# Kernel tuning notes

Measured on AMD Instinct MI355X. Metric: run time of the kernel, lower is better.

Reference implementation:

```python
import jax, jax.numpy as jnp
import numpy as np

D = 256    # lstm_encoder_size
B = 1024   # batch (number of agents/trajectories)
T = 512    # prediction horizon (recurrence steps)
EPS = 1e-5


def setup_inputs() -> dict:
    key = jax.random.key(0)
    k = jax.random.split(key, 10)
    s = 1.0 / np.sqrt(D)
    return {
        "KS_ALL": jax.random.normal(k[0], (1, B, D), jnp.float32),
        "next_vf": jax.random.normal(k[1], (B, T), jnp.float32),
        # Koopman operators (torch Linear stores [out, in]; no bias)
        "A_w": jax.random.normal(k[2], (D, D), jnp.float32) * (0.4 * s),  # contractive
        "B_w": jax.random.normal(k[3], (D, 1), jnp.float32) * s,
        # decoder params (liner_dec=False)
        "W0": jax.random.normal(k[4], (2 * D, D), jnp.float32) * s,
        "b0": jnp.zeros((2 * D,), jnp.float32),
        "W1": jax.random.normal(k[5], (D, 2 * D), jnp.float32) / np.sqrt(2.0 * D),
        "b1": jnp.zeros((D,), jnp.float32),
        "ln_g": jnp.ones((D,), jnp.float32),
        "ln_b": jnp.zeros((D,), jnp.float32),
        "W2": jax.random.normal(k[6], (D, D), jnp.float32) * s,
        "b2": jnp.zeros((D,), jnp.float32),
        "W3": jax.random.normal(k[7], (3, D), jnp.float32) * s,
        "b3": jnp.zeros((3,), jnp.float32),
    }


def _layer_norm(x, g, b):
    mu = jnp.mean(x, axis=-1, keepdims=True)
    var = jnp.var(x, axis=-1, keepdims=True)
    return (x - mu) * jax.lax.rsqrt(var + EPS) * g + b


def reference(KS_ALL, next_vf, A_w, B_w, W0, b0, W1, b1, ln_g, ln_b, W2, b2, W3, b3):
    # train_flag=True -> use only the first time slice of KS_ALL
    ks0 = KS_ALL[0]                 # [B, D]
    u = next_vf.T                   # [T, B] time-major, matches permute(1,0,2)
    b_vec = B_w[:, 0]               # [D]  (Linear(1, D) on scalar input)

    def step(ks, u_t):
        ks_new = ks @ A_w.T + u_t[:, None] * b_vec[None, :]  # [B, D]
        return ks_new, ks_new

    _, ks_seq = jax.lax.scan(step, ks0, u)                   # [T, B, D]
    KS_pre = jnp.concatenate([ks0[None], ks_seq], axis=0)    # [T+1, B, D]

    # nonlinear decoder (eval mode: dropout is identity; use_elu=True)
    s1 = jnp.tanh(KS_pre @ W0.T + b0)          # [T+1, B, 2D]
    s2 = jnp.tanh(s1 @ W1.T + b1)              # [T+1, B, D]
    s2 = _layer_norm(KS_pre + s2, ln_g, ln_b)  # AddAndNorm
    s3 = jax.nn.elu(s2 @ W2.T + b2)
    OS = s3 @ W3.T + b3                        # [T+1, B, 3]
    return KS_pre, OS
```

## Files before the change

### kernel.cpp

```cpp
#include <hip/hip_runtime.h>

typedef unsigned short u16;
typedef __attribute__((ext_vector_type(8))) short bf16x8;
typedef __attribute__((ext_vector_type(4))) short bf16x4;
typedef __attribute__((ext_vector_type(4))) float f32x4;

#define MFMA16(a, b, c) __builtin_amdgcn_mfma_f32_16x16x32_bf16((a), (b), (c), 0, 0, 0)

#define OFF_U8   0
#define U8_CPY   598016
#define OFF_KS0  4784128
#define OFF_W0   5046272
#define OFF_W1   5177344
#define OFF_W2   5308416
#define OFF_CRT  5373952
#define OFF_P    5390336
#define OS_OFF   134479872

__device__ __forceinline__ u16 f2bf(float f) {
  union { float f; unsigned int i; } v; v.f = f;
  return (u16)((v.i + 0x7fffu + ((v.i >> 16) & 1u)) >> 16);
}
__device__ __forceinline__ float bf2f(u16 u) {
  union { unsigned int i; float f; } v; v.i = ((unsigned int)u) << 16;
  return v.f;
}
__device__ __forceinline__ float fast_tanh(float x) {
  float e = __expf(2.0f * x);
  return 1.0f - __fdividef(2.0f, e + 1.0f);
}

__global__ void k_prep(const float* __restrict__ KS_ALL, const float* __restrict__ next_vf,
                       const float* __restrict__ A_w, const float* __restrict__ W0,
                       const float* __restrict__ W1, const float* __restrict__ W2,
                       u16* __restrict__ ws) {
  int idx = blockIdx.x * 256 + threadIdx.x;
  if (idx < 4784128) {
    int p = idx / U8_CPY;
    int rem = idx - p * U8_CPY;
    int b = rem / 584;
    int c = rem - b * 584;
    int col = c + p;
    ws[OFF_U8 + idx] = (col >= 64 && col < 576) ? f2bf(next_vf[b * 512 + col - 64]) : (u16)0;
    return;
  }
  idx -= 4784128;
  if (idx < 262144) { ws[OFF_KS0 + idx] = f2bf(KS_ALL[idx]); return; }
  idx -= 262144;
  if (idx < 131072) { ws[OFF_W0 + idx] = f2bf(W0[idx]); return; }
  idx -= 131072;
  if (idx < 131072) { ws[OFF_W1 + idx] = f2bf(W1[idx]); return; }
  idx -= 131072;
  if (idx < 65536)  { ws[OFF_W2 + idx] = f2bf(W2[idx]); return; }
  idx -= 65536;
  if (idx < 65536) {
    int r = idx >> 8, c = idx & 255;
    ws[OFF_P + idx] = (r == c) ? (u16)0x3F80 : (u16)0;
    ws[OFF_P + 65536 + idx] = f2bf(A_w[idx]);
  }
}

__global__ __launch_bounds__(512) void k_pow(u16* __restrict__ ws, int s) {
  const u16* P = ws + OFF_P;
  int j = blockIdx.y + 1;
  int mh = blockIdx.x;
  int lane = threadIdx.x & 63, w = threadIdx.x >> 6;
  int wm = w >> 2, wn = w & 3;
  int lg = lane >> 4, ll = lane & 15;
  const u16* Am = P + s * 65536;
  const u16* Bm = P + j * 65536;
  f32x4 acc[4][4];
  f32x4 z = {0.f, 0.f, 0.f, 0.f};
#pragma unroll
  for (int mi = 0; mi < 4; ++mi)
#pragma unroll
    for (int ni = 0; ni < 4; ++ni) acc[mi][ni] = z;
#pragma unroll
  for (int ks = 0; ks < 8; ++ks) {
    bf16x8 a[4], b[4];
    int kk = ks * 32 + lg * 8;
#pragma unroll
    for (int mi = 0; mi < 4; ++mi) {
      int row = mh * 128 + wm * 64 + mi * 16 + ll;
      a[mi] = *(const bf16x8*)(Am + row * 256 + kk);
    }
#pragma unroll
    for (int ni = 0; ni < 4; ++ni) {
      int col = wn * 64 + ni * 16 + ll;
#pragma unroll
      for (int e = 0; e < 8; ++e) b[ni][e] = (short)Bm[(kk + e) * 256 + col];
    }
#pragma unroll
    for (int mi = 0; mi < 4; ++mi)
#pragma unroll
      for (int ni = 0; ni < 4; ++ni) acc[mi][ni] = MFMA16(a[mi], b[ni], acc[mi][ni]);
  }
  u16* Pd = ws + OFF_P + (s + j) * 65536;
#pragma unroll
  for (int mi = 0; mi < 4; ++mi)
#pragma unroll
    for (int ni = 0; ni < 4; ++ni)
#pragma unroll
      for (int r = 0; r < 4; ++r) {
        int row = mh * 128 + wm * 64 + mi * 16 + lg * 4 + r;
        int col = wn * 64 + ni * 16 + ll;
        Pd[row * 256 + col] = f2bf(acc[mi][ni][r]);
      }
}

__global__ void k_crevt(const float* __restrict__ B_w, u16* __restrict__ ws) {
  int s = blockIdx.x;
  int n = threadIdx.x;
  const u16* Pr = ws + OFF_P + (63 - s) * 65536 + n * 256;
  float acc = 0.f;
  for (int k = 0; k < 256; ++k) acc += bf2f(Pr[k]) * B_w[k];
  ws[OFF_CRT + n * 64 + s] = f2bf(acc);
}

__global__ __launch_bounds__(512) void k_ks(const u16* __restrict__ ws, float* __restrict__ out) {
  __shared__ __align__(16) float Hf[32 * 260];
  const int t  = blockIdx.y;
  const int R0 = blockIdx.x * 64;
  const int tid = threadIdx.x;
  const int lane = tid & 63, w = tid >> 6;
  const int lg = lane >> 4, ll = lane & 15;
  f32x4 z = {0.f, 0.f, 0.f, 0.f};

  f32x4 acc[4][2];
#pragma unroll
  for (int mi = 0; mi < 4; ++mi)
#pragma unroll
    for (int ni = 0; ni < 2; ++ni) acc[mi][ni] = z;
  {
    const u16* CrevT = ws + OFF_CRT;
    const u16* u8b = ws + OFF_U8 + (size_t)(t & 7) * U8_CPY + (t & ~7);
#pragma unroll
    for (int ksu = 0; ksu < 2; ++ksu) {
      bf16x8 au[4];
#pragma unroll
      for (int mi = 0; mi < 4; ++mi)
        au[mi] = *(const bf16x8*)(u8b + (R0 + mi * 16 + ll) * 584 + ksu * 32 + lg * 8);
#pragma unroll
      for (int ni = 0; ni < 2; ++ni) {
        int n = w * 32 + ni * 16 + ll;
        bf16x8 bfr = *(const bf16x8*)(CrevT + n * 64 + ksu * 32 + lg * 8);
#pragma unroll
        for (int mi = 0; mi < 4; ++mi) acc[mi][ni] = MFMA16(au[mi], bfr, acc[mi][ni]);
      }
    }
    if (t < 64) {
      const u16* Pt = ws + OFF_P + t * 65536;
      const u16* ks0b = ws + OFF_KS0;
#pragma unroll
      for (int ks = 0; ks < 8; ++ks) {
        bf16x8 a[4], b[2];
#pragma unroll
        for (int mi = 0; mi < 4; ++mi)
          a[mi] = *(const bf16x8*)(ks0b + (R0 + mi * 16 + ll) * 256 + ks * 32 + lg * 8);
#pragma unroll
        for (int ni = 0; ni < 2; ++ni)
          b[ni] = *(const bf16x8*)(Pt + (w * 32 + ni * 16 + ll) * 256 + ks * 32 + lg * 8);
#pragma unroll
        for (int mi = 0; mi < 4; ++mi)
#pragma unroll
          for (int ni = 0; ni < 2; ++ni) acc[mi][ni] = MFMA16(a[mi], b[ni], acc[mi][ni]);
      }
    }
  }
#pragma unroll 1
  for (int p = 0; p < 2; ++p) {
#pragma unroll
    for (int mi2 = 0; mi2 < 2; ++mi2) {
      int mi = p * 2 + mi2;
#pragma unroll
      for (int ni = 0; ni < 2; ++ni)
#pragma unroll
        for (int r = 0; r < 4; ++r)
          Hf[(mi2 * 16 + lg * 4 + r) * 260 + w * 32 + ni * 16 + ll] = acc[mi][ni][r];
    }
    __syncthreads();
    float* ob = out + (size_t)t * 262144 + (size_t)(R0 + p * 32) * 256;
#pragma unroll
    for (int it = 0; it < 4; ++it) {
      int idx = it * 512 + tid;
      int row = idx >> 6, c4 = idx & 63;
      f32x4 v = *(const f32x4*)(Hf + row * 260 + c4 * 4);
      __builtin_nontemporal_store(v, (f32x4*)(ob + row * 256 + c4 * 4));
    }
    __syncthreads();
  }
}

__global__ __launch_bounds__(512) void k_mlp(const u16* __restrict__ ws,
                                             const float* __restrict__ outf,
                                             const float* __restrict__ b0,
                                             const float* __restrict__ b1,
                                             const float* __restrict__ lng,
                                             const float* __restrict__ lnb,
                                             const float* __restrict__ b2,
                                             const float* __restrict__ W3,
                                             const float* __restrict__ b3,
                                             float* __restrict__ out) {
  __shared__ __align__(16) u16 Xb[16896];
  __shared__ __align__(16) u16 Hs[8448];
  __shared__ float par[2308];
  __shared__ float osb[208];
  float* pb0 = par;
  float* pb1 = par + 512;
  float* pg  = par + 768;
  float* pbt = par + 1024;
  float* pb2 = par + 1280;
  float* pW3 = par + 1536;
  float* pb3 = par + 2304;
  const int t  = blockIdx.y;
  const int R0 = blockIdx.x * 64;
  const int tid = threadIdx.x;
  const int lane = tid & 63, w = tid >> 6;
  const int lg = lane >> 4, ll = lane & 15;
  f32x4 z = {0.f, 0.f, 0.f, 0.f};

  pb0[tid] = b0[tid];
  if (tid < 256) { pb1[tid] = b1[tid]; pg[tid] = lng[tid]; pbt[tid] = lnb[tid]; pb2[tid] = b2[tid]; }
  if (tid < 512) pW3[tid] = W3[tid];
  if (tid < 256) pW3[512 + tid] = W3[512 + tid];
  if (tid < 4) pb3[tid] = (tid < 3) ? b3[tid] : 0.f;

  {
    const float* xs = outf + (size_t)t * 262144 + (size_t)R0 * 256;
#pragma unroll
    for (int it = 0; it < 8; ++it) {
      int idx = it * 512 + tid;
      int row = idx >> 6, c4 = idx & 63;
      f32x4 v = __builtin_nontemporal_load((const f32x4*)(xs + row * 256 + c4 * 4));
      bf16x4 h;
#pragma unroll
      for (int e = 0; e < 4; ++e) h[e] = (short)f2bf(v[e]);
      int byt = (((row << 9) + ((c4 >> 1) << 4)) ^ ((row & 7) << 4)) + ((c4 & 1) << 3);
      *(bf16x4*)(Xb + (byt >> 1)) = h;
    }
  }
  __syncthreads();

  const u16* W0b = ws + OFF_W0;
  const u16* W1b = ws + OFF_W1;
  f32x4 accL2[4][2];
#pragma unroll
  for (int mi = 0; mi < 4; ++mi)
#pragma unroll
    for (int ni = 0; ni < 2; ++ni) accL2[mi][ni] = z;
  const int colL1 = w * 16 + ll;
#pragma unroll 1
  for (int q = 0; q < 4; ++q) {
    f32x4 accQ[4];
#pragma unroll
    for (int mi = 0; mi < 4; ++mi) accQ[mi] = z;
#pragma unroll
    for (int ks = 0; ks < 8; ++ks) {
      bf16x8 b = *(const bf16x8*)(W0b + (q * 128 + colL1) * 256 + ks * 32 + lg * 8);
#pragma unroll
      for (int mi = 0; mi < 4; ++mi) {
        int rl = mi * 16 + ll;
        int byt = ((rl << 9) + ks * 64 + (lg << 4)) ^ ((rl & 7) << 4);
        bf16x8 a = *(const bf16x8*)(Xb + (byt >> 1));
        accQ[mi] = MFMA16(a, b, accQ[mi]);
      }
    }
#pragma unroll
    for (int mi = 0; mi < 4; ++mi)
#pragma unroll
      for (int r = 0; r < 4; ++r) {
        int rl2 = mi * 16 + lg * 4 + r;
        float v = fast_tanh(accQ[mi][r] + pb0[q * 128 + colL1]);
        int byt = ((rl2 << 8) + (colL1 << 1)) ^ ((rl2 & 7) << 4);
        Hs[byt >> 1] = f2bf(v);
      }
    __syncthreads();
#pragma unroll
    for (int ks2 = 0; ks2 < 4; ++ks2) {
      bf16x8 bf0 = *(const bf16x8*)(W1b + (w * 32 + ll) * 512 + q * 128 + ks2 * 32 + lg * 8);
      bf16x8 bf1 = *(const bf16x8*)(W1b + (w * 32 + 16 + ll) * 512 + q * 128 + ks2 * 32 + lg * 8);
#pragma unroll
      for (int mi = 0; mi < 4; ++mi) {
        int rl = mi * 16 + ll;
        int byt = ((rl << 8) + ks2 * 64 + (lg << 4)) ^ ((rl & 7) << 4);
        bf16x8 a = *(const bf16x8*)(Hs + (byt >> 1));
        accL2[mi][0] = MFMA16(a, bf0, accL2[mi][0]);
        accL2[mi][1] = MFMA16(a, bf1, accL2[mi][1]);
      }
    }
    __syncthreads();
  }

#pragma unroll
  for (int mi = 0; mi < 4; ++mi)
#pragma unroll
    for (int ni = 0; ni < 2; ++ni)
#pragma unroll
      for (int r = 0; r < 4; ++r) {
        int rl = mi * 16 + lg * 4 + r;
        int col = w * 32 + ni * 16 + ll;
        int bx = ((rl << 9) + (col << 1)) ^ ((rl & 7) << 4);
        float v = bf2f(Xb[bx >> 1]) + fast_tanh(accL2[mi][ni][r] + pb1[col]);
        Xb[bx >> 1] = f2bf(v);
      }
  __syncthreads();

  {
    int row = tid >> 3, jq = tid & 7;
    bf16x8 chv[4];
    int byts[4];
#pragma unroll
    for (int q = 0; q < 4; ++q) {
      byts[q] = ((row << 9) + ((jq * 32 + q * 8) << 1)) ^ ((row & 7) << 4);
      chv[q] = *(const bf16x8*)(Xb + (byts[q] >> 1));
    }
    float s = 0.f, ss = 0.f;
#pragma unroll
    for (int q = 0; q < 4; ++q)
#pragma unroll
      for (int e = 0; e < 8; ++e) { float v = bf2f((u16)chv[q][e]); s += v; ss += v * v; }
    s += __shfl_xor(s, 1);  s += __shfl_xor(s, 2);  s += __shfl_xor(s, 4);
    ss += __shfl_xor(ss, 1); ss += __shfl_xor(ss, 2); ss += __shfl_xor(ss, 4);
    float mu = s * 0.00390625f;
    float var = ss * 0.00390625f - mu * mu;
    float rstd = rsqrtf(var + 1e-5f);
#pragma unroll
    for (int q = 0; q < 4; ++q) {
      bf16x8 o;
#pragma unroll
      for (int e = 0; e < 8; ++e) {
        int col = jq * 32 + q * 8 + e;
        float v = (bf2f((u16)chv[q][e]) - mu) * rstd * pg[col] + pbt[col];
        o[e] = (short)f2bf(v);
      }
      *(bf16x8*)(Xb + (byts[q] >> 1)) = o;
    }
  }
  __syncthreads();

  f32x4 a3[4][2];
#pragma unroll
  for (int mi = 0; mi < 4; ++mi)
#pragma unroll
    for (int ni = 0; ni < 2; ++ni) a3[mi][ni] = z;
  {
    const u16* W2b = ws + OFF_W2;
#pragma unroll
    for (int ks = 0; ks < 8; ++ks) {
      bf16x8 bf0 = *(const bf16x8*)(W2b + (w * 32 + ll) * 256 + ks * 32 + lg * 8);
      bf16x8 bf1 = *(const bf16x8*)(W2b + (w * 32 + 16 + ll) * 256 + ks * 32 + lg * 8);
#pragma unroll
      for (int mi = 0; mi < 4; ++mi) {
        int rl = mi * 16 + ll;
        int byt = ((rl << 9) + ks * 64 + (lg << 4)) ^ ((rl & 7) << 4);
        bf16x8 a = *(const bf16x8*)(Xb + (byt >> 1));
        a3[mi][0] = MFMA16(a, bf0, a3[mi][0]);
        a3[mi][1] = MFMA16(a, bf1, a3[mi][1]);
      }
    }
  }
  __syncthreads();
#pragma unroll
  for (int mi = 0; mi < 4; ++mi)
#pragma unroll
    for (int ni = 0; ni < 2; ++ni)
#pragma unroll
      for (int r = 0; r < 4; ++r) {
        int rl = mi * 16 + lg * 4 + r;
        int col = w * 32 + ni * 16 + ll;
        float v = a3[mi][ni][r] + pb2[col];
        v = v > 0.f ? v : (__expf(v) - 1.f);
        Xb[rl * 264 + col] = f2bf(v);
      }
  __syncthreads();

  {
    int row = tid >> 3, jq = tid & 7;
    const u16* xr = Xb + row * 264 + jq * 32;
    float d0 = 0.f, d1 = 0.f, d2 = 0.f;
#pragma unroll
    for (int q = 0; q < 4; ++q) {
      bf16x8 c = *(const bf16x8*)(xr + q * 8);
#pragma unroll
      for (int e = 0; e < 8; ++e) {
        float v = bf2f((u16)c[e]);
        int col = jq * 32 + q * 8 + e;
        d0 += v * pW3[col]; d1 += v * pW3[256 + col]; d2 += v * pW3[512 + col];
      }
    }
    d0 += __shfl_xor(d0, 1); d0 += __shfl_xor(d0, 2); d0 += __shfl_xor(d0, 4);
    d1 += __shfl_xor(d1, 1); d1 += __shfl_xor(d1, 2); d1 += __shfl_xor(d1, 4);
    d2 += __shfl_xor(d2, 1); d2 += __shfl_xor(d2, 2); d2 += __shfl_xor(d2, 4);
    if (jq == 0) {
      osb[row * 3]     = d0 + pb3[0];
      osb[row * 3 + 1] = d1 + pb3[1];
      osb[row * 3 + 2] = d2 + pb3[2];
    }
  }
  __syncthreads();
  if (tid < 48) {
    f32x4 v = *(const f32x4*)(osb + tid * 4);
    __builtin_nontemporal_store(v, (f32x4*)(out + OS_OFF + (size_t)t * 3072 + (size_t)R0 * 3 + tid * 4));
  }
}

extern "C" void kernel_launch(void* const* d_in, const int* in_sizes, int n_in,
                              void* d_out, int out_size, void* d_ws, size_t ws_size,
                              hipStream_t stream) {
  const float* KS_ALL  = (const float*)d_in[0];
  const float* next_vf = (const float*)d_in[1];
  const float* A_w     = (const float*)d_in[2];
  const float* B_w     = (const float*)d_in[3];
  const float* W0      = (const float*)d_in[4];
  const float* b0      = (const float*)d_in[5];
  const float* W1      = (const float*)d_in[6];
  const float* b1      = (const float*)d_in[7];
  const float* lng     = (const float*)d_in[8];
  const float* lnb     = (const float*)d_in[9];
  const float* W2      = (const float*)d_in[10];
  const float* b2      = (const float*)d_in[11];
  const float* W3      = (const float*)d_in[12];
  const float* b3      = (const float*)d_in[13];
  u16* ws = (u16*)d_ws;
  float* out = (float*)d_out;

  k_prep<<<21248, 256, 0, stream>>>(KS_ALL, next_vf, A_w, W0, W1, W2, ws);
  for (int s = 1; s <= 32; s <<= 1)
    k_pow<<<dim3(2, s), 512, 0, stream>>>(ws, s);
  k_crevt<<<64, 256, 0, stream>>>(B_w, ws);

  k_ks<<<dim3(16, 513), 512, 0, stream>>>(ws, out);
  k_mlp<<<dim3(16, 513), 512, 0, stream>>>(ws, out, b0, b1, lng, lnb, b2, W3, b3, out);
}
```

Measured before the change: 1.503 ms.

## Double k_mlp block to 1024 threads, halving per-wave columns and L1 chunks

The decoder MLP kernel now launches 1024 threads (16 waves) per 64-row tile instead of 512. Each wave owns 16 output columns instead of 32, and the hidden layer is processed in two 256-wide chunks instead of four 128-wide chunks, with a larger shared staging buffer. The LayerNorm and final projection reductions are respread over 16 lanes per row. The aim is more waves in flight per tile to hide latency and fewer barrier rounds, at the cost of fewer accumulators per wave, more shared memory and possibly lower block occupancy per CU.

```diff
diff --git a/kernel.cpp b/kernel.cpp
--- a/kernel.cpp
+++ b/kernel.cpp
@@ -191,18 +191,18 @@
   }
 }
 
-__global__ __launch_bounds__(512) void k_mlp(const u16* __restrict__ ws,
-                                             const float* __restrict__ outf,
-                                             const float* __restrict__ b0,
-                                             const float* __restrict__ b1,
-                                             const float* __restrict__ lng,
-                                             const float* __restrict__ lnb,
-                                             const float* __restrict__ b2,
-                                             const float* __restrict__ W3,
-                                             const float* __restrict__ b3,
-                                             float* __restrict__ out) {
+__global__ __launch_bounds__(1024) void k_mlp(const u16* __restrict__ ws,
+                                              const float* __restrict__ outf,
+                                              const float* __restrict__ b0,
+                                              const float* __restrict__ b1,
+                                              const float* __restrict__ lng,
+                                              const float* __restrict__ lnb,
+                                              const float* __restrict__ b2,
+                                              const float* __restrict__ W3,
+                                              const float* __restrict__ b3,
+                                              float* __restrict__ out) {
   __shared__ __align__(16) u16 Xb[16896];
-  __shared__ __align__(16) u16 Hs[8448];
+  __shared__ __align__(16) u16 Hs[16384];
   __shared__ float par[2308];
   __shared__ float osb[208];
   float* pb0 = par;
@@ -217,19 +217,19 @@
   const int tid = threadIdx.x;
   const int lane = tid & 63, w = tid >> 6;
   const int lg = lane >> 4, ll = lane & 15;
+  const int colW = w * 16 + ll;
   f32x4 z = {0.f, 0.f, 0.f, 0.f};
 
-  pb0[tid] = b0[tid];
+  if (tid < 512) pb0[tid] = b0[tid];
   if (tid < 256) { pb1[tid] = b1[tid]; pg[tid] = lng[tid]; pbt[tid] = lnb[tid]; pb2[tid] = b2[tid]; }
-  if (tid < 512) pW3[tid] = W3[tid];
-  if (tid < 256) pW3[512 + tid] = W3[512 + tid];
+  if (tid < 768) pW3[tid] = W3[tid];
   if (tid < 4) pb3[tid] = (tid < 3) ? b3[tid] : 0.f;
 
   {
     const float* xs = outf + (size_t)t * 262144 + (size_t)R0 * 256;
 #pragma unroll
-    for (int it = 0; it < 8; ++it) {
-      int idx = it * 512 + tid;
+    for (int it = 0; it < 4; ++it) {
+      int idx = it * 1024 + tid;
       int row = idx >> 6, c4 = idx & 63;
       f32x4 v = __builtin_nontemporal_load((const f32x4*)(xs + row * 256 + c4 * 4));
       bf16x4 h;
@@ -243,20 +243,17 @@
 
   const u16* W0b = ws + OFF_W0;
   const u16* W1b = ws + OFF_W1;
-  f32x4 accL2[4][2];
-#pragma unroll
-  for (int mi = 0; mi < 4; ++mi)
-#pragma unroll
-    for (int ni = 0; ni < 2; ++ni) accL2[mi][ni] = z;
-  const int colL1 = w * 16 + ll;
+  f32x4 accL2[4];
+#pragma unroll
+  for (int mi = 0; mi < 4; ++mi) accL2[mi] = z;
 #pragma unroll 1
-  for (int q = 0; q < 4; ++q) {
+  for (int q = 0; q < 2; ++q) {
     f32x4 accQ[4];
 #pragma unroll
     for (int mi = 0; mi < 4; ++mi) accQ[mi] = z;
 #pragma unroll
     for (int ks = 0; ks < 8; ++ks) {
-      bf16x8 b = *(const bf16x8*)(W0b + (q * 128 + colL1) * 256 + ks * 32 + lg * 8);
+      bf16x8 b = *(const bf16x8*)(W0b + (q * 256 + colW) * 256 + ks * 32 + lg * 8);
 #pragma unroll
       for (int mi = 0; mi < 4; ++mi) {
         int rl = mi * 16 + ll;
@@ -270,22 +267,20 @@
 #pragma unroll
       for (int r = 0; r < 4; ++r) {
         int rl2 = mi * 16 + lg * 4 + r;
-        float v = fast_tanh(accQ[mi][r] + pb0[q * 128 + colL1]);
-        int byt = ((rl2 << 8) + (colL1 << 1)) ^ ((rl2 & 7) << 4);
+        float v = fast_tanh(accQ[mi][r] + pb0[q * 256 + colW]);
+        int byt = ((rl2 << 9) + (colW << 1)) ^ ((rl2 & 7) << 4);
         Hs[byt >> 1] = f2bf(v);
       }
     __syncthreads();
 #pragma unroll
-    for (int ks2 = 0; ks2 < 4; ++ks2) {
-      bf16x8 bf0 = *(const bf16x8*)(W1b + (w * 32 + ll) * 512 + q * 128 + ks2 * 32 + lg * 8);
-      bf16x8 bf1 = *(const bf16x8*)(W1b + (w * 32 + 16 + ll) * 512 + q * 128 + ks2 * 32 + lg * 8);
+    for (int ks = 0; ks < 8; ++ks) {
+      bf16x8 b = *(const bf16x8*)(W1b + colW * 512 + q * 256 + ks * 32 + lg * 8);
 #pragma unroll
       for (int mi = 0; mi < 4; ++mi) {
         int rl = mi * 16 + ll;
-        int byt = ((rl << 8) + ks2 * 64 + (lg << 4)) ^ ((rl & 7) << 4);
+        int byt = ((rl << 9) + ks * 64 + (lg << 4)) ^ ((rl & 7) << 4);
         bf16x8 a = *(const bf16x8*)(Hs + (byt >> 1));
-        accL2[mi][0] = MFMA16(a, bf0, accL2[mi][0]);
-        accL2[mi][1] = MFMA16(a, bf1, accL2[mi][1]);
+        accL2[mi] = MFMA16(a, b, accL2[mi]);
       }
     }
     __syncthreads();
@@ -294,68 +289,59 @@
 #pragma unroll
   for (int mi = 0; mi < 4; ++mi)
 #pragma unroll
-    for (int ni = 0; ni < 2; ++ni)
-#pragma unroll
-      for (int r = 0; r < 4; ++r) {
-        int rl = mi * 16 + lg * 4 + r;
-        int col = w * 32 + ni * 16 + ll;
-        int bx = ((rl << 9) + (col << 1)) ^ ((rl & 7) << 4);
-        float v = bf2f(Xb[bx >> 1]) + fast_tanh(accL2[mi][ni][r] + pb1[col]);
-        Xb[bx >> 1] = f2bf(v);
-      }
+    for (int r = 0; r < 4; ++r) {
+      int rl = mi * 16 + lg * 4 + r;
+      int bx = ((rl << 9) + (colW << 1)) ^ ((rl & 7) << 4);
+      float v = bf2f(Xb[bx >> 1]) + fast_tanh(accL2[mi][r] + pb1[colW]);
+      Xb[bx >> 1] = f2bf(v);
+    }
   __syncthreads();
 
   {
-    int row = tid >> 3, jq = tid & 7;
-    bf16x8 chv[4];
-    int byts[4];
-#pragma unroll
-    for (int q = 0; q < 4; ++q) {
-      byts[q] = ((row << 9) + ((jq * 32 + q * 8) << 1)) ^ ((row & 7) << 4);
-      chv[q] = *(const bf16x8*)(Xb + (byts[q] >> 1));
-    }
+    int row = tid >> 4, jq = tid & 15;
+    bf16x8 chv[2];
+    int byt0 = ((row << 9) + ((jq * 16) << 1)) ^ ((row & 7) << 4);
+    int byt1 = ((row << 9) + ((jq * 16 + 8) << 1)) ^ ((row & 7) << 4);
+    chv[0] = *(const bf16x8*)(Xb + (byt0 >> 1));
+    chv[1] = *(const bf16x8*)(Xb + (byt1 >> 1));
     float s = 0.f, ss = 0.f;
 #pragma unroll
-    for (int q = 0; q < 4; ++q)
+    for (int q = 0; q < 2; ++q)
 #pragma unroll
       for (int e = 0; e < 8; ++e) { float v = bf2f((u16)chv[q][e]); s += v; ss += v * v; }
-    s += __shfl_xor(s, 1);  s += __shfl_xor(s, 2);  s += __shfl_xor(s, 4);
-    ss += __shfl_xor(ss, 1); ss += __shfl_xor(ss, 2); ss += __shfl_xor(ss, 4);
+    s += __shfl_xor(s, 1);  s += __shfl_xor(s, 2);  s += __shfl_xor(s, 4);  s += __shfl_xor(s, 8);
+    ss += __shfl_xor(ss, 1); ss += __shfl_xor(ss, 2); ss += __shfl_xor(ss, 4); ss += __shfl_xor(ss, 8);
     float mu = s * 0.00390625f;
     float var = ss * 0.00390625f - mu * mu;
     float rstd = rsqrtf(var + 1e-5f);
 #pragma unroll
-    for (int q = 0; q < 4; ++q) {
+    for (int q = 0; q < 2; ++q) {
       bf16x8 o;
 #pragma unroll
       for (int e = 0; e < 8; ++e) {
-        int col = jq * 32 + q * 8 + e;
+        int col = jq * 16 + q * 8 + e;
         float v = (bf2f((u16)chv[q][e]) - mu) * rstd * pg[col] + pbt[col];
         o[e] = (short)f2bf(v);
       }
-      *(bf16x8*)(Xb + (byts[q] >> 1)) = o;
-    }
-  }
-  __syncthreads();
-
-  f32x4 a3[4][2];
-#pragma unroll
-  for (int mi = 0; mi < 4; ++mi)
-#pragma unroll
-    for (int ni = 0; ni < 2; ++ni) a3[mi][ni] = z;
+      *(bf16x8*)(Xb + ((q ? byt1 : byt0) >> 1)) = o;
+    }
+  }
+  __syncthreads();
+
+  f32x4 a3[4];
+#pragma unroll
+  for (int mi = 0; mi < 4; ++mi) a3[mi] = z;
   {
     const u16* W2b = ws + OFF_W2;
 #pragma unroll
     for (int ks = 0; ks < 8; ++ks) {
-      bf16x8 bf0 = *(const bf16x8*)(W2b + (w * 32 + ll) * 256 + ks * 32 + lg * 8);
-      bf16x8 bf1 = *(const bf16x8*)(W2b + (w * 32 + 16 + ll) * 256 + ks * 32 + lg * 8);
+      bf16x8 b = *(const bf16x8*)(W2b + colW * 256 + ks * 32 + lg * 8);
 #pragma unroll
       for (int mi = 0; mi < 4; ++mi) {
         int rl = mi * 16 + ll;
         int byt = ((rl << 9) + ks * 64 + (lg << 4)) ^ ((rl & 7) << 4);
         bf16x8 a = *(const bf16x8*)(Xb + (byt >> 1));
-        a3[mi][0] = MFMA16(a, bf0, a3[mi][0]);
-        a3[mi][1] = MFMA16(a, bf1, a3[mi][1]);
+        a3[mi] = MFMA16(a, b, a3[mi]);
       }
     }
   }
@@ -363,34 +349,31 @@
 #pragma unroll
   for (int mi = 0; mi < 4; ++mi)
 #pragma unroll
-    for (int ni = 0; ni < 2; ++ni)
-#pragma unroll
-      for (int r = 0; r < 4; ++r) {
-        int rl = mi * 16 + lg * 4 + r;
-        int col = w * 32 + ni * 16 + ll;
-        float v = a3[mi][ni][r] + pb2[col];
-        v = v > 0.f ? v : (__expf(v) - 1.f);
-        Xb[rl * 264 + col] = f2bf(v);
-      }
+    for (int r = 0; r < 4; ++r) {
+      int rl = mi * 16 + lg * 4 + r;
+      float v = a3[mi][r] + pb2[colW];
+      v = v > 0.f ? v : (__expf(v) - 1.f);
+      Xb[rl * 264 + colW] = f2bf(v);
+    }
   __syncthreads();
 
   {
-    int row = tid >> 3, jq = tid & 7;
-    const u16* xr = Xb + row * 264 + jq * 32;
+    int row = tid >> 4, jq = tid & 15;
+    const u16* xr = Xb + row * 264 + jq * 16;
     float d0 = 0.f, d1 = 0.f, d2 = 0.f;
 #pragma unroll
-    for (int q = 0; q < 4; ++q) {
+    for (int q = 0; q < 2; ++q) {
       bf16x8 c = *(const bf16x8*)(xr + q * 8);
 #pragma unroll
       for (int e = 0; e < 8; ++e) {
         float v = bf2f((u16)c[e]);
-        int col = jq * 32 + q * 8 + e;
+        int col = jq * 16 + q * 8 + e;
         d0 += v * pW3[col]; d1 += v * pW3[256 + col]; d2 += v * pW3[512 + col];
       }
     }
-    d0 += __shfl_xor(d0, 1); d0 += __shfl_xor(d0, 2); d0 += __shfl_xor(d0, 4);
-    d1 += __shfl_xor(d1, 1); d1 += __shfl_xor(d1, 2); d1 += __shfl_xor(d1, 4);
-    d2 += __shfl_xor(d2, 1); d2 += __shfl_xor(d2, 2); d2 += __shfl_xor(d2, 4);
+    d0 += __shfl_xor(d0, 1); d0 += __shfl_xor(d0, 2); d0 += __shfl_xor(d0, 4); d0 += __shfl_xor(d0, 8);
+    d1 += __shfl_xor(d1, 1); d1 += __shfl_xor(d1, 2); d1 += __shfl_xor(d1, 4); d1 += __shfl_xor(d1, 8);
+    d2 += __shfl_xor(d2, 1); d2 += __shfl_xor(d2, 2); d2 += __shfl_xor(d2, 4); d2 += __shfl_xor(d2, 8);
     if (jq == 0) {
       osb[row * 3]     = d0 + pb3[0];
       osb[row * 3 + 1] = d1 + pb3[1];
@@ -430,5 +413,5 @@
   k_crevt<<<64, 256, 0, stream>>>(B_w, ws);
 
   k_ks<<<dim3(16, 513), 512, 0, stream>>>(ws, out);
-  k_mlp<<<dim3(16, 513), 512, 0, stream>>>(ws, out, b0, b1, lng, lnb, b2, W3, b3, out);
-}
+  k_mlp<<<dim3(16, 513), 1024, 0, stream>>>(ws, out, b0, b1, lng, lnb, b2, W3, b3, out);
+}
```

New measurement: 1.453 ms. -3.3%, faster.

## Fuse first decoder layer into KS kernel and chunk time to stream hidden activations

Applied to the files above, without the earlier changes.

The KS computation kernel now also runs the first decoder GEMM and tanh from the bf16 KS tile held in shared memory. It writes the bf16 hidden layer to a workspace buffer instead of having the MLP kernel re-read the fp32 KS output. The second kernel handles layers 2-4 from that buffer. The work is split into four time chunks so the intermediate buffer stays small and may stay cache-resident between the paired kernels. The cost is heavier per-block shared memory, extra launches, and a round trip of the 512-wide hidden layer through global memory.

```diff
diff --git a/kernel.cpp b/kernel.cpp
--- a/kernel.cpp
+++ b/kernel.cpp
@@ -15,6 +15,7 @@
 #define OFF_W2   5308416
 #define OFF_CRT  5373952
 #define OFF_P    5390336
+#define OFF_H1   9650176
 #define OS_OFF   134479872
 
 __device__ __forceinline__ u16 f2bf(float f) {
@@ -117,15 +118,25 @@
   ws[OFF_CRT + n * 64 + s] = f2bf(acc);
 }
 
-__global__ __launch_bounds__(512) void k_ks(const u16* __restrict__ ws, float* __restrict__ out) {
-  __shared__ __align__(16) float Hf[32 * 260];
-  const int t  = blockIdx.y;
+__global__ __launch_bounds__(512) void k_ksl1(const u16* __restrict__ ws,
+                                              const float* __restrict__ b0,
+                                              u16* __restrict__ h1,
+                                              float* __restrict__ out, int t0) {
+  __shared__ __align__(16) u16 Xb[16896];
+  __shared__ __align__(16) unsigned char Hraw[33792];
+  __shared__ float pb0s[512];
+  float* Hf = (float*)Hraw;
+  u16* Hb = (u16*)Hraw;
+  const int by = blockIdx.y;
+  const int t  = t0 + by;
   const int R0 = blockIdx.x * 64;
   const int tid = threadIdx.x;
   const int lane = tid & 63, w = tid >> 6;
   const int lg = lane >> 4, ll = lane & 15;
   f32x4 z = {0.f, 0.f, 0.f, 0.f};
 
+  pb0s[tid] = b0[tid];
+
   f32x4 acc[4][2];
 #pragma unroll
   for (int mi = 0; mi < 4; ++mi)
@@ -167,6 +178,19 @@
       }
     }
   }
+
+#pragma unroll
+  for (int mi = 0; mi < 4; ++mi)
+#pragma unroll
+    for (int ni = 0; ni < 2; ++ni)
+#pragma unroll
+      for (int r = 0; r < 4; ++r) {
+        int rl = mi * 16 + lg * 4 + r;
+        int col = w * 32 + ni * 16 + ll;
+        int byt = ((rl << 9) + (col << 1)) ^ ((rl & 7) << 4);
+        Xb[byt >> 1] = f2bf(acc[mi][ni][r]);
+      }
+
 #pragma unroll 1
   for (int p = 0; p < 2; ++p) {
 #pragma unroll
@@ -189,131 +213,150 @@
     }
     __syncthreads();
   }
-}
-
-__global__ __launch_bounds__(512) void k_mlp(const u16* __restrict__ ws,
+
+  const u16* W0b = ws + OFF_W0;
+#pragma unroll 1
+  for (int nh = 0; nh < 2; ++nh) {
+    f32x4 acc2[4][2];
+#pragma unroll
+    for (int mi = 0; mi < 4; ++mi)
+#pragma unroll
+      for (int ni = 0; ni < 2; ++ni) acc2[mi][ni] = z;
+#pragma unroll
+    for (int ks = 0; ks < 8; ++ks) {
+      bf16x8 b[2];
+#pragma unroll
+      for (int ni = 0; ni < 2; ++ni) {
+        int n = nh * 256 + w * 32 + ni * 16 + ll;
+        b[ni] = *(const bf16x8*)(W0b + n * 256 + ks * 32 + lg * 8);
+      }
+#pragma unroll
+      for (int mi = 0; mi < 4; ++mi) {
+        int rl = mi * 16 + ll;
+        int byt = ((rl << 9) + ks * 64 + (lg << 4)) ^ ((rl & 7) << 4);
+        bf16x8 a = *(const bf16x8*)(Xb + (byt >> 1));
+#pragma unroll
+        for (int ni = 0; ni < 2; ++ni) acc2[mi][ni] = MFMA16(a, b[ni], acc2[mi][ni]);
+      }
+    }
+#pragma unroll
+    for (int mi = 0; mi < 4; ++mi)
+#pragma unroll
+      for (int ni = 0; ni < 2; ++ni)
+#pragma unroll
+        for (int r = 0; r < 4; ++r) {
+          int rl = mi * 16 + lg * 4 + r;
+          int col = w * 32 + ni * 16 + ll;
+          Hb[rl * 264 + col] = f2bf(fast_tanh(acc2[mi][ni][r] + pb0s[nh * 256 + col]));
+        }
+    __syncthreads();
+    u16* hd = h1 + ((size_t)(by * 1024 + R0)) * 512 + nh * 256;
+#pragma unroll
+    for (int it = 0; it < 4; ++it) {
+      int idx = it * 512 + tid;
+      int row = idx >> 5, cq = idx & 31;
+      bf16x8 v = *(const bf16x8*)(Hb + row * 264 + cq * 8);
+      __builtin_nontemporal_store(v, (bf16x8*)(hd + row * 512 + cq * 8));
+    }
+    __syncthreads();
+  }
+}
+
+__global__ __launch_bounds__(512) void k_l23(const u16* __restrict__ ws,
                                              const float* __restrict__ outf,
-                                             const float* __restrict__ b0,
                                              const float* __restrict__ b1,
                                              const float* __restrict__ lng,
                                              const float* __restrict__ lnb,
                                              const float* __restrict__ b2,
                                              const float* __restrict__ W3,
                                              const float* __restrict__ b3,
-                                             float* __restrict__ out) {
-  __shared__ __align__(16) u16 Xb[16896];
-  __shared__ __align__(16) u16 Hs[8448];
-  __shared__ float par[2308];
+                                             const u16* __restrict__ h1,
+                                             float* __restrict__ out, int t0) {
+  __shared__ __align__(16) u16 Hs[16896];
+  __shared__ __align__(16) u16 Rb[16896];
+  __shared__ float par[1796];
   __shared__ float osb[208];
-  float* pb0 = par;
-  float* pb1 = par + 512;
-  float* pg  = par + 768;
-  float* pbt = par + 1024;
-  float* pb2 = par + 1280;
-  float* pW3 = par + 1536;
-  float* pb3 = par + 2304;
-  const int t  = blockIdx.y;
+  float* pb1 = par;
+  float* pg  = par + 256;
+  float* pbt = par + 512;
+  float* pb2 = par + 768;
+  float* pW3 = par + 1024;
+  float* pb3 = par + 1792;
+  const int by = blockIdx.y;
+  const int t  = t0 + by;
   const int R0 = blockIdx.x * 64;
   const int tid = threadIdx.x;
   const int lane = tid & 63, w = tid >> 6;
   const int lg = lane >> 4, ll = lane & 15;
   f32x4 z = {0.f, 0.f, 0.f, 0.f};
 
-  pb0[tid] = b0[tid];
   if (tid < 256) { pb1[tid] = b1[tid]; pg[tid] = lng[tid]; pbt[tid] = lnb[tid]; pb2[tid] = b2[tid]; }
   if (tid < 512) pW3[tid] = W3[tid];
   if (tid < 256) pW3[512 + tid] = W3[512 + tid];
   if (tid < 4) pb3[tid] = (tid < 3) ? b3[tid] : 0.f;
 
-  {
-    const float* xs = outf + (size_t)t * 262144 + (size_t)R0 * 256;
-#pragma unroll
-    for (int it = 0; it < 8; ++it) {
+  f32x4 accL2[4][2];
+#pragma unroll
+  for (int mi = 0; mi < 4; ++mi)
+#pragma unroll
+    for (int ni = 0; ni < 2; ++ni) accL2[mi][ni] = z;
+
+  const u16* W1b = ws + OFF_W1;
+  const u16* h1b = h1 + ((size_t)(by * 1024 + R0)) * 512;
+#pragma unroll 1
+  for (int kh = 0; kh < 2; ++kh) {
+#pragma unroll
+    for (int it = 0; it < 4; ++it) {
       int idx = it * 512 + tid;
-      int row = idx >> 6, c4 = idx & 63;
-      f32x4 v = __builtin_nontemporal_load((const f32x4*)(xs + row * 256 + c4 * 4));
-      bf16x4 h;
-#pragma unroll
-      for (int e = 0; e < 4; ++e) h[e] = (short)f2bf(v[e]);
-      int byt = (((row << 9) + ((c4 >> 1) << 4)) ^ ((row & 7) << 4)) + ((c4 & 1) << 3);
-      *(bf16x4*)(Xb + (byt >> 1)) = h;
-    }
-  }
-  __syncthreads();
-
-  const u16* W0b = ws + OFF_W0;
-  const u16* W1b = ws + OFF_W1;
-  f32x4 accL2[4][2];
-#pragma unroll
-  for (int mi = 0; mi < 4; ++mi)
-#pragma unroll
-    for (int ni = 0; ni < 2; ++ni) accL2[mi][ni] = z;
-  const int colL1 = w * 16 + ll;
-#pragma unroll 1
-  for (int q = 0; q < 4; ++q) {
-    f32x4 accQ[4];
-#pragma unroll
-    for (int mi = 0; mi < 4; ++mi) accQ[mi] = z;
+      int row = idx >> 5, cq = idx & 31;
+      bf16x8 v = __builtin_nontemporal_load((const bf16x8*)(h1b + row * 512 + kh * 256 + cq * 8));
+      int byt = ((row << 9) + (cq << 4)) ^ ((row & 7) << 4);
+      *(bf16x8*)(Hs + (byt >> 1)) = v;
+    }
+    __syncthreads();
 #pragma unroll
     for (int ks = 0; ks < 8; ++ks) {
-      bf16x8 b = *(const bf16x8*)(W0b + (q * 128 + colL1) * 256 + ks * 32 + lg * 8);
+      bf16x8 b[2];
+#pragma unroll
+      for (int ni = 0; ni < 2; ++ni) {
+        int n = w * 32 + ni * 16 + ll;
+        b[ni] = *(const bf16x8*)(W1b + n * 512 + kh * 256 + ks * 32 + lg * 8);
+      }
 #pragma unroll
       for (int mi = 0; mi < 4; ++mi) {
         int rl = mi * 16 + ll;
         int byt = ((rl << 9) + ks * 64 + (lg << 4)) ^ ((rl & 7) << 4);
-        bf16x8 a = *(const bf16x8*)(Xb + (byt >> 1));
-        accQ[mi] = MFMA16(a, b, accQ[mi]);
-      }
-    }
-#pragma unroll
-    for (int mi = 0; mi < 4; ++mi)
-#pragma unroll
-      for (int r = 0; r < 4; ++r) {
-        int rl2 = mi * 16 + lg * 4 + r;
-        float v = fast_tanh(accQ[mi][r] + pb0[q * 128 + colL1]);
-        int byt = ((rl2 << 8) + (colL1 << 1)) ^ ((rl2 & 7) << 4);
-        Hs[byt >> 1] = f2bf(v);
-      }
-    __syncthreads();
-#pragma unroll
-    for (int ks2 = 0; ks2 < 4; ++ks2) {
-      bf16x8 bf0 = *(const bf16x8*)(W1b + (w * 32 + ll) * 512 + q * 128 + ks2 * 32 + lg * 8);
-      bf16x8 bf1 = *(const bf16x8*)(W1b + (w * 32 + 16 + ll) * 512 + q * 128 + ks2 * 32 + lg * 8);
-#pragma unroll
-      for (int mi = 0; mi < 4; ++mi) {
-        int rl = mi * 16 + ll;
-        int byt = ((rl << 8) + ks2 * 64 + (lg << 4)) ^ ((rl & 7) << 4);
         bf16x8 a = *(const bf16x8*)(Hs + (byt >> 1));
-        accL2[mi][0] = MFMA16(a, bf0, accL2[mi][0]);
-        accL2[mi][1] = MFMA16(a, bf1, accL2[mi][1]);
-      }
-    }
-    __syncthreads();
-  }
-
-#pragma unroll
-  for (int mi = 0; mi < 4; ++mi)
-#pragma unroll
-    for (int ni = 0; ni < 2; ++ni)
-#pragma unroll
-      for (int r = 0; r < 4; ++r) {
-        int rl = mi * 16 + lg * 4 + r;
-        int col = w * 32 + ni * 16 + ll;
-        int bx = ((rl << 9) + (col << 1)) ^ ((rl & 7) << 4);
-        float v = bf2f(Xb[bx >> 1]) + fast_tanh(accL2[mi][ni][r] + pb1[col]);
-        Xb[bx >> 1] = f2bf(v);
-      }
+#pragma unroll
+        for (int ni = 0; ni < 2; ++ni) accL2[mi][ni] = MFMA16(a, b[ni], accL2[mi][ni]);
+      }
+    }
+    __syncthreads();
+  }
+
+  {
+    const float* xs = outf + (size_t)t * 262144 + (size_t)R0 * 256;
+#pragma unroll
+    for (int mi = 0; mi < 4; ++mi)
+#pragma unroll
+      for (int ni = 0; ni < 2; ++ni)
+#pragma unroll
+        for (int r = 0; r < 4; ++r) {
+          int rl = mi * 16 + lg * 4 + r;
+          int col = w * 32 + ni * 16 + ll;
+          float xv = __builtin_nontemporal_load(xs + rl * 256 + col);
+          float v = xv + fast_tanh(accL2[mi][ni][r] + pb1[col]);
+          Rb[rl * 264 + col] = f2bf(v);
+        }
+  }
   __syncthreads();
 
   {
     int row = tid >> 3, jq = tid & 7;
+    u16* hr = Rb + row * 264 + jq * 32;
     bf16x8 chv[4];
-    int byts[4];
-#pragma unroll
-    for (int q = 0; q < 4; ++q) {
-      byts[q] = ((row << 9) + ((jq * 32 + q * 8) << 1)) ^ ((row & 7) << 4);
-      chv[q] = *(const bf16x8*)(Xb + (byts[q] >> 1));
-    }
+#pragma unroll
+    for (int q = 0; q < 4; ++q) chv[q] = *(const bf16x8*)(hr + q * 8);
     float s = 0.f, ss = 0.f;
 #pragma unroll
     for (int q = 0; q < 4; ++q)
@@ -333,50 +376,52 @@
         float v = (bf2f((u16)chv[q][e]) - mu) * rstd * pg[col] + pbt[col];
         o[e] = (short)f2bf(v);
       }
-      *(bf16x8*)(Xb + (byts[q] >> 1)) = o;
+      *(bf16x8*)(hr + q * 8) = o;
     }
   }
   __syncthreads();
 
-  f32x4 a3[4][2];
-#pragma unroll
-  for (int mi = 0; mi < 4; ++mi)
-#pragma unroll
-    for (int ni = 0; ni < 2; ++ni) a3[mi][ni] = z;
   {
     const u16* W2b = ws + OFF_W2;
+    f32x4 a3[4][2];
+#pragma unroll
+    for (int mi = 0; mi < 4; ++mi)
+#pragma unroll
+      for (int ni = 0; ni < 2; ++ni) a3[mi][ni] = z;
 #pragma unroll
     for (int ks = 0; ks < 8; ++ks) {
-      bf16x8 bf0 = *(const bf16x8*)(W2b + (w * 32 + ll) * 256 + ks * 32 + lg * 8);
-      bf16x8 bf1 = *(const bf16x8*)(W2b + (w * 32 + 16 + ll) * 256 + ks * 32 + lg * 8);
+      bf16x8 b[2];
+#pragma unroll
+      for (int ni = 0; ni < 2; ++ni) {
+        int n = w * 32 + ni * 16 + ll;
+        b[ni] = *(const bf16x8*)(W2b + n * 256 + ks * 32 + lg * 8);
+      }
 #pragma unroll
       for (int mi = 0; mi < 4; ++mi) {
         int rl = mi * 16 + ll;
-        int byt = ((rl << 9) + ks * 64 + (lg << 4)) ^ ((rl & 7) << 4);
-        bf16x8 a = *(const bf16x8*)(Xb + (byt >> 1));
-        a3[mi][0] = MFMA16(a, bf0, a3[mi][0]);
-        a3[mi][1] = MFMA16(a, bf1, a3[mi][1]);
-      }
-    }
-  }
-  __syncthreads();
-#pragma unroll
-  for (int mi = 0; mi < 4; ++mi)
-#pragma unroll
-    for (int ni = 0; ni < 2; ++ni)
-#pragma unroll
-      for (int r = 0; r < 4; ++r) {
-        int rl = mi * 16 + lg * 4 + r;
-        int col = w * 32 + ni * 16 + ll;
-        float v = a3[mi][ni][r] + pb2[col];
-        v = v > 0.f ? v : (__expf(v) - 1.f);
-        Xb[rl * 264 + col] = f2bf(v);
-      }
+        bf16x8 a = *(const bf16x8*)(Rb + rl * 264 + ks * 32 + lg * 8);
+#pragma unroll
+        for (int ni = 0; ni < 2; ++ni) a3[mi][ni] = MFMA16(a, b[ni], a3[mi][ni]);
+      }
+    }
+#pragma unroll
+    for (int mi = 0; mi < 4; ++mi)
+#pragma unroll
+      for (int ni = 0; ni < 2; ++ni)
+#pragma unroll
+        for (int r = 0; r < 4; ++r) {
+          int rl = mi * 16 + lg * 4 + r;
+          int col = w * 32 + ni * 16 + ll;
+          float v = a3[mi][ni][r] + pb2[col];
+          v = v > 0.f ? v : (__expf(v) - 1.f);
+          Hs[rl * 264 + col] = f2bf(v);
+        }
+  }
   __syncthreads();
 
   {
     int row = tid >> 3, jq = tid & 7;
-    const u16* xr = Xb + row * 264 + jq * 32;
+    const u16* xr = Hs + row * 264 + jq * 32;
     float d0 = 0.f, d1 = 0.f, d2 = 0.f;
 #pragma unroll
     for (int q = 0; q < 4; ++q) {
@@ -429,6 +474,11 @@
     k_pow<<<dim3(2, s), 512, 0, stream>>>(ws, s);
   k_crevt<<<64, 256, 0, stream>>>(B_w, ws);
 
-  k_ks<<<dim3(16, 513), 512, 0, stream>>>(ws, out);
-  k_mlp<<<dim3(16, 513), 512, 0, stream>>>(ws, out, b0, b1, lng, lnb, b2, W3, b3, out);
-}
+  u16* h1 = ws + OFF_H1;
+  const int t0s[4] = {0, 129, 257, 385};
+  const int nts[4] = {129, 128, 128, 128};
+  for (int c = 0; c < 4; ++c) {
+    k_ksl1<<<dim3(16, nts[c]), 512, 0, stream>>>(ws, b0, h1, out, t0s[c]);
+    k_l23<<<dim3(16, nts[c]), 512, 0, stream>>>(ws, out, b1, lng, lnb, b2, W3, b3, h1, out, t0s[c]);
+  }
+}
```

Measured after the change: 1.373 ms. -8.7%, faster.
